# Performance work log

Hardware: AMD Instinct MI355X
Metric: run time of the kernel (lower is better)

The kernel has to match this reference:

```python
import jax, jax.numpy as jnp
import numpy as np
import math

NHID = 32
FEAT_SIZE = 32
FEAT_SIZE_LIST = [16, 32, 32, 32]
SEQ_LEN = len(FEAT_SIZE_LIST)   # 4
N_EDGE_LABELS = 3
NLAYERS = 2
N_GRAPHS = 64
FINAL = SEQ_LEN * NHID          # 128


def _pos_enc(max_len, dim):
    pe = np.zeros((max_len, dim), dtype=np.float32)
    pos = np.arange(max_len, dtype=np.float32)[:, None]
    div = np.exp(np.arange(0, dim, 2, dtype=np.float32) * (-math.log(10000.0) / dim))
    pe[:, 0::2] = np.sin(pos * div)
    pe[:, 1::2] = np.cos(pos * div)
    return jnp.asarray(pe)


def _feature_attention(x, wqkv, w1, b1, w2, b2):
    # x: [N, S*NHID] -> attention over the S feature 'tokens' per node
    N, D = x.shape
    S = D // NHID
    xr = x.reshape(N, S, NHID)
    qkv = jnp.einsum('nsf,fh->nsh', xr, wqkv)          # [N,S,3*NHID]
    q, k, v = jnp.split(qkv, 3, axis=-1)
    att = jax.nn.softmax(jnp.einsum('nsh,nth->nst', q, k) / jnp.sqrt(jnp.asarray(NHID, x.dtype)), axis=-1)
    y = jnp.einsum('nst,nth->nsh', att, v)             # [N,S,NHID]
    y = y + (jax.nn.relu(y @ w1 + b1) @ w2 + b2)       # residual FFN
    return y.reshape(N, -1)


def setup_inputs() -> dict:
    key = jax.random.key(0)
    ks = jax.random.split(key, 16)
    N = 100000
    E = 800000
    inp = {
        'x': jax.random.normal(ks[0], (N, 112), dtype=jnp.float32),
        'edge_index0': jax.random.randint(ks[1], (2, E), 0, N),
        'edge_index1': jax.random.randint(ks[2], (2, E), 0, N),
        'edge_index2': jax.random.randint(ks[3], (2, E), 0, N),
        'batch': jnp.sort(jax.random.randint(ks[4], (N,), 0, N_GRAPHS)),
    }
    s = 0.05
    # FeatureLinear encoder (bias-free)
    inp['W_emb'] = jax.random.normal(ks[5], (FEAT_SIZE, NHID), dtype=jnp.float32) * s
    # Per layer: [root, conv0, conv1, conv2] FeatureAttention params, stacked
    A = 1 + N_EDGE_LABELS
    inp['qkv'] = jax.random.normal(ks[6], (NLAYERS, A, NHID, 3 * NHID), dtype=jnp.float32) * s
    inp['ffn_w1'] = jax.random.normal(ks[7], (NLAYERS, A, NHID, NHID), dtype=jnp.float32) * s
    inp['ffn_b1'] = jnp.zeros((NLAYERS, A, NHID), dtype=jnp.float32)
    inp['ffn_w2'] = jax.random.normal(ks[8], (NLAYERS, A, NHID, NHID), dtype=jnp.float32) * s
    inp['ffn_b2'] = jnp.zeros((NLAYERS, A, NHID), dtype=jnp.float32)
    # Heuristic decoder MLP: 128 -> 128 -> 1
    inp['mlp_w1'] = jax.random.normal(ks[9], (FINAL, FINAL), dtype=jnp.float32) * s
    inp['mlp_b1'] = jnp.zeros((FINAL,), dtype=jnp.float32)
    inp['mlp_w2'] = jax.random.normal(ks[10], (FINAL, 1), dtype=jnp.float32) * s
    inp['mlp_b2'] = jnp.zeros((1,), dtype=jnp.float32)
    return inp


def reference(x, edge_index0, edge_index1, edge_index2, batch,
              W_emb, qkv, ffn_w1, ffn_b1, ffn_w2, ffn_b2,
              mlp_w1, mlp_b1, mlp_w2, mlp_b2):
    N = x.shape[0]
    edge_indices = [edge_index0, edge_index1, edge_index2]

    # padding: split by feat_size_list, right-pad each chunk to FEAT_SIZE
    offs = np.cumsum(FEAT_SIZE_LIST)[:-1].tolist()
    chunks = jnp.split(x, offs, axis=1)
    padded = [jnp.pad(c, ((0, 0), (0, FEAT_SIZE - c.shape[1]))) for c in chunks]
    h = jnp.concatenate(padded, axis=1)                       # [N, SEQ_LEN*FEAT_SIZE]

    # sinusoidal positional encoding over the SEQ_LEN feature tokens
    pe = _pos_enc(10, FEAT_SIZE)[:SEQ_LEN]                    # [SEQ_LEN, FEAT_SIZE]
    h = (h.reshape(N, SEQ_LEN, FEAT_SIZE) + pe[None]).reshape(N, -1)

    # FeatureLinear encoder: per-token linear FEAT_SIZE -> NHID
    h = jnp.einsum('nsf,fh->nsh', h.reshape(N, SEQ_LEN, FEAT_SIZE), W_emb).reshape(N, -1)

    # RGNN layers: root attention + per-edge-label attention->scatter-sum
    for l in range(NLAYERS):
        x_out = _feature_attention(h, qkv[l, 0], ffn_w1[l, 0], ffn_b1[l, 0], ffn_w2[l, 0], ffn_b2[l, 0])
        for e in range(N_EDGE_LABELS):
            a = e + 1
            xt = _feature_attention(h, qkv[l, a], ffn_w1[l, a], ffn_b1[l, a], ffn_w2[l, a], ffn_b2[l, a])
            src, dst = edge_indices[e][0], edge_indices[e][1]
            x_out = x_out + jax.ops.segment_sum(xt[src], dst, num_segments=N)
        h = jax.nn.relu(x_out)

    # global mean pool over graphs
    sums = jax.ops.segment_sum(h, batch, num_segments=N_GRAPHS)
    cnts = jax.ops.segment_sum(jnp.ones((N,), h.dtype), batch, num_segments=N_GRAPHS)
    g = sums / jnp.maximum(cnts, 1.0)[:, None]                # [G, FINAL]

    # heuristic decoder
    out = jax.nn.relu(g @ mlp_w1 + mlp_b1) @ mlp_w2 + mlp_b2  # [G, 1]
    return out.squeeze(1)                                     # [G]
```

## Files before the change

kernel.cpp:

```cpp
#include <hip/hip_runtime.h>
#include <hip/hip_bf16.h>
#include <cstdint>
#include <cstddef>


typedef __attribute__((ext_vector_type(8))) short bf16x8;
typedef __attribute__((ext_vector_type(4))) float f32x4;
typedef __attribute__((ext_vector_type(2))) float f32x2;

#if defined(__has_builtin)
#if __has_builtin(__builtin_amdgcn_cvt_pk_fp8_f32) && __has_builtin(__builtin_amdgcn_cvt_pk_f32_fp8)
#define HW_FP8 1
#endif
#if __has_builtin(__builtin_amdgcn_cvt_pk_bf16_f32)
#define HW_PKBF16 1
#endif
#endif

__device__ inline short f2bf(float f) {
    union { float f; unsigned u; } v; v.f = f;
    unsigned r = (v.u + 0x7FFFu + ((v.u >> 16) & 1u)) >> 16;
    return (short)r;
}
__device__ inline float bf2f(unsigned short b) {
    union { unsigned u; float f; } v; v.u = ((unsigned)b) << 16;
    return v.f;
}
#ifdef HW_PKBF16
typedef __attribute__((ext_vector_type(2))) __bf16 bf16x2_t;
__device__ inline unsigned pk2(float a, float b) {
    union { bf16x2_t v; unsigned u; } c;
    c.v = __builtin_amdgcn_cvt_pk_bf16_f32(a, b);
    return c.u;
}
#else
__device__ inline unsigned pk2(float a, float b) {
    unsigned ua = __float_as_uint(a) + 0x8000u;
    unsigned ub = __float_as_uint(b) + 0x8000u;
    return __builtin_amdgcn_perm(ub, ua, 0x07060302u);
}
#endif

#ifndef HW_FP8
__device__ inline unsigned char f2fp8_sw(float f) {
    unsigned s = (__float_as_uint(f) >> 31) & 1u;
    float a = fminf(fabsf(f), 448.f);
    unsigned char bits;
    if (a < 0.015625f) {
        bits = (unsigned char)__float2int_rn(a * 512.f);
    } else {
        int e; float m = frexpf(a, &e);
        int mf = __float2int_rn(m * 16.f);
        if (mf == 16) { mf = 8; e += 1; }
        int ef = e - 1 + 7;
        if (ef > 15) { ef = 15; mf = 14; }
        bits = (unsigned char)((ef << 3) | (mf & 7));
    }
    return (unsigned char)((s << 7) | bits);
}
__device__ inline float fp82f_sw(unsigned b) {
    int s = (b >> 7) & 1, e = (b >> 3) & 15, m = b & 7;
    float v = e ? ldexpf((float)(8 + m), e - 10) : ldexpf((float)m, -9);
    return s ? -v : v;
}
#endif

__device__ inline unsigned pk4fp8(float v0, float v1, float v2, float v3) {
#ifdef HW_FP8
    int w = __builtin_amdgcn_cvt_pk_fp8_f32(v0, v1, 0, false);
    w = __builtin_amdgcn_cvt_pk_fp8_f32(v2, v3, w, true);
    return (unsigned)w;
#else
    return (unsigned)f2fp8_sw(v0) | ((unsigned)f2fp8_sw(v1) << 8) |
           ((unsigned)f2fp8_sw(v2) << 16) | ((unsigned)f2fp8_sw(v3) << 24);
#endif
}
__device__ inline float2 up2fp8(unsigned short raw) {
#ifdef HW_FP8
    f32x2 f = __builtin_amdgcn_cvt_pk_f32_fp8((int)(unsigned)raw, false);
    return make_float2(f[0], f[1]);
#else
    return make_float2(fp82f_sw(raw & 0xffu), fp82f_sw((raw >> 8) & 0xffu));
#endif
}

__global__ __launch_bounds__(64) void wprep_kernel(
    const float* __restrict__ qkv, const float* __restrict__ fw1,
    const float* __restrict__ fw2, unsigned short* __restrict__ wpack,
    int* __restrict__ bcnt, int* __restrict__ gres,
    float* __restrict__ gsum, float* __restrict__ gcnt)
{
    const int pi = blockIdx.x;
    const int lane = threadIdx.x;
    const int gid = pi * 64 + lane;
    for (int i = gid; i < 256; i += 512) { bcnt[i] = 0; gres[i] = 0; }
    for (int i = gid; i < 64 * 128; i += 512) gsum[i] = 0.f;
    if (gid < 64) gcnt[gid] = 0.f;

    const int q = lane >> 4, m = lane & 15;
    const float* Wq = qkv + (size_t)pi * 32 * 96;
    const float* W1 = fw1 + (size_t)pi * 32 * 32;
    const float* W2 = fw2 + (size_t)pi * 32 * 32;
    unsigned short* dst = wpack + (size_t)pi * 10 * 64 * 8;
#pragma unroll
    for (int ci = 0; ci < 6; ++ci)
#pragma unroll
        for (int j = 0; j < 8; ++j)
            dst[(ci * 64 + lane) * 8 + j] =
                (unsigned short)f2bf(Wq[(q * 8 + j) * 96 + ci * 16 + m]);
#pragma unroll
    for (int t = 0; t < 2; ++t)
#pragma unroll
        for (int j = 0; j < 8; ++j) {
            dst[((6 + t) * 64 + lane) * 8 + j] =
                (unsigned short)f2bf(W1[(q * 8 + j) * 32 + t * 16 + m]);
            dst[((8 + t) * 64 + lane) * 8 + j] =
                (unsigned short)f2bf(W2[(q * 8 + j) * 32 + t * 16 + m]);
        }
}

__global__ __launch_bounds__(128) void enc_kernel(
    const float* __restrict__ x, const float* __restrict__ Wemb,
    unsigned short* __restrict__ h, int N)
{
    __shared__ float sxr[8 * 112];
    __shared__ float spe[128];
    __shared__ float sW[1024];
    const int t = threadIdx.x;
    const int n0 = blockIdx.x * 8;

    {
        int s = t >> 5, f = t & 31;
        int i2 = f >> 1;
        float div = __expf(-(float)(2 * i2) * (logf(10000.0f) / 32.0f));
        float ang = (float)s * div;
        spe[t] = (f & 1) ? cosf(ang) : sinf(ang);
    }
    for (int i = t; i < 1024; i += 128) sW[i] = Wemb[i];
    for (int i = t; i < 8 * 112; i += 128) {
        int n = n0 + i / 112;
        sxr[i] = (n < N) ? x[(size_t)n0 * 112 + i] : 0.f;
    }
    __syncthreads();

    const int ts = t >> 5, c = t & 31;
    const int offs_[4] = {0, 16, 48, 80};
    const int lens_[4] = {16, 32, 32, 32};
    const int off = offs_[ts], len = lens_[ts];

    float acc[8];
#pragma unroll
    for (int i = 0; i < 8; ++i) acc[i] = 0.f;
    float pw = 0.f;
    for (int f = 0; f < 32; ++f) {
        float wv = sW[f * 32 + c];
        float pv = spe[ts * 32 + f];
        pw += pv * wv;
        if (f < len) {
#pragma unroll
            for (int i = 0; i < 8; ++i) acc[i] += sxr[i * 112 + off + f] * wv;
        }
    }
#pragma unroll
    for (int i = 0; i < 8; ++i) {
        int n = n0 + i;
        if (n < N)
            h[(size_t)n * 128 + ts * 32 + c] = (unsigned short)f2bf(acc[i] + pw);
    }
}

#define ATT_WAVES 4
#define WLDS 5376

__global__ __launch_bounds__(256, 3) void attn4_kernel(
    const unsigned short* __restrict__ in,
    unsigned short* __restrict__ outR, unsigned char* __restrict__ out3,
    const unsigned short* __restrict__ wpack,
    const float* __restrict__ fb1, const float* __restrict__ fb2,
    int pibase, int N)
{
    __shared__ char smem[ATT_WAVES * 2 * WLDS];
    const int lane = threadIdx.x & 63;
    const int wave = threadIdx.x >> 6;
    const int q = lane >> 4;
    const int m = lane & 15;

    char* wb0 = smem + wave * (2 * WLDS);

#pragma unroll
    for (int u = 0; u < 2; ++u) {
        int* p32 = (int*)(wb0 + u * WLDS + 4096);
        for (int i = lane; i < 320; i += 64) p32[i] = 0;
    }

    const f32x4 zf = {0.f, 0.f, 0.f, 0.f};
    const int pi = pibase + wave;
    unsigned char* out8 = out3 + (size_t)(wave - 1) * N * 128;

    bf16x8 wqkv[6], w1f[2], w2f[2];
    float b1r[2][4], b2r[2][4];
    {
        const unsigned short* wp = wpack + ((size_t)pi * 10 * 64 + lane) * 8;
#pragma unroll
        for (int ci = 0; ci < 6; ++ci)
            wqkv[ci] = *(const bf16x8*)(wp + ci * 64 * 8);
#pragma unroll
        for (int t = 0; t < 2; ++t) {
            w1f[t] = *(const bf16x8*)(wp + (6 + t) * 64 * 8);
            w2f[t] = *(const bf16x8*)(wp + (8 + t) * 64 * 8);
#pragma unroll
            for (int r = 0; r < 4; ++r) {
                b1r[t][r] = fb1[pi * 32 + 16 * t + q * 4 + r];
                b2r[t][r] = fb2[pi * 32 + 16 * t + q * 4 + r];
            }
        }
    }

    const int nsuper = (N + 7) >> 3;
    for (int stile = blockIdx.x; stile < nsuper; stile += gridDim.x) {
        const int n0 = stile * 8;

        bf16x8 ax[2];
#pragma unroll
        for (int u = 0; u < 2; ++u) {
            bf16x8 a = {0, 0, 0, 0, 0, 0, 0, 0};
            int nm = n0 + 4 * u + (m >> 2);
            if (nm < N)
                a = *(const bf16x8*)(in + (size_t)(n0 + 4 * u) * 128 + m * 32 + q * 8);
            ax[u] = a;
        }

#pragma unroll
        for (int u = 0; u < 2; ++u) {
            char* wbu = wb0 + u * WLDS;
            short* Qb = (short*)(wbu);
            short* Kb = (short*)(wbu + 1280);
            short* VT = (short*)(wbu + 2560);
            short* Pb = (short*)(wbu + 4096);

            f32x4 aQ[2], aK[2], aV[2];
#pragma unroll
            for (int t = 0; t < 2; ++t) {
                aQ[t] = __builtin_amdgcn_mfma_f32_16x16x32_bf16(wqkv[t],     ax[u], zf, 0, 0, 0);
                aK[t] = __builtin_amdgcn_mfma_f32_16x16x32_bf16(wqkv[2 + t], ax[u], zf, 0, 0, 0);
                aV[t] = __builtin_amdgcn_mfma_f32_16x16x32_bf16(ax[u], wqkv[4 + t], zf, 0, 0, 0);
            }
#pragma unroll
            for (int t = 0; t < 2; ++t) {
                uint2 dq, dk, dv;
                dq.x = pk2(aQ[t][0], aQ[t][1]); dq.y = pk2(aQ[t][2], aQ[t][3]);
                dk.x = pk2(aK[t][0], aK[t][1]); dk.y = pk2(aK[t][2], aK[t][3]);
                dv.x = pk2(aV[t][0], aV[t][1]); dv.y = pk2(aV[t][2], aV[t][3]);
                *(uint2*)(Qb + m * 40 + 16 * t + q * 4) = dq;
                *(uint2*)(Kb + m * 40 + 16 * t + q * 4) = dk;
                *(uint2*)(VT + (16 * t + m) * 24 + q * 4) = dv;
            }

            bf16x8 aKf = *(const bf16x8*)(Kb + m * 40 + q * 8);
            bf16x8 bQf = *(const bf16x8*)(Qb + m * 40 + q * 8);
            f32x4 st = __builtin_amdgcn_mfma_f32_16x16x32_bf16(aKf, bQf, zf, 0, 0, 0);

            float v0 = st[0] * 0.1767766952966369f;
            float v1 = st[1] * 0.1767766952966369f;
            float v2 = st[2] * 0.1767766952966369f;
            float v3 = st[3] * 0.1767766952966369f;
            float mx = fmaxf(fmaxf(v0, v1), fmaxf(v2, v3));
            float e0 = __expf(v0 - mx), e1 = __expf(v1 - mx);
            float e2 = __expf(v2 - mx), e3 = __expf(v3 - mx);
            float inv = 1.0f / (e0 + e1 + e2 + e3);
            if (q == (m >> 2)) {
                uint2 dp;
                dp.x = pk2(e0 * inv, e1 * inv);
                dp.y = pk2(e2 * inv, e3 * inv);
                *(uint2*)(Pb + m * 40 + q * 4) = dp;
            }

            f32x4 y[2];
#pragma unroll
            for (int t = 0; t < 2; ++t) {
                bf16x8 aVf = {0, 0, 0, 0, 0, 0, 0, 0};
                bf16x8 bPf = {0, 0, 0, 0, 0, 0, 0, 0};
                if (q < 2) {
                    aVf = *(const bf16x8*)(VT + (16 * t + m) * 24 + q * 8);
                    bPf = *(const bf16x8*)(Pb + m * 40 + q * 8);
                }
                y[t] = __builtin_amdgcn_mfma_f32_16x16x32_bf16(aVf, bPf, zf, 0, 0, 0);
            }
#pragma unroll
            for (int t = 0; t < 2; ++t) {
                uint2 dy;
                dy.x = pk2(y[t][0], y[t][1]); dy.y = pk2(y[t][2], y[t][3]);
                *(uint2*)(Qb + m * 40 + 16 * t + q * 4) = dy;
            }

            bf16x8 bY = *(const bf16x8*)(Qb + m * 40 + q * 8);
            f32x4 z1[2];
#pragma unroll
            for (int t = 0; t < 2; ++t)
                z1[t] = __builtin_amdgcn_mfma_f32_16x16x32_bf16(w1f[t], bY, zf, 0, 0, 0);
#pragma unroll
            for (int t = 0; t < 2; ++t) {
                uint2 dz;
                dz.x = pk2(fmaxf(z1[t][0] + b1r[t][0], 0.f),
                           fmaxf(z1[t][1] + b1r[t][1], 0.f));
                dz.y = pk2(fmaxf(z1[t][2] + b1r[t][2], 0.f),
                           fmaxf(z1[t][3] + b1r[t][3], 0.f));
                *(uint2*)(Kb + m * 40 + 16 * t + q * 4) = dz;
            }

            bf16x8 bZ = *(const bf16x8*)(Kb + m * 40 + q * 8);
            f32x4 o[2];
#pragma unroll
            for (int t = 0; t < 2; ++t)
                o[t] = __builtin_amdgcn_mfma_f32_16x16x32_bf16(w2f[t], bZ, zf, 0, 0, 0);

            if (n0 + 4 * u + (m >> 2) < N) {
                if (wave == 0) {
#pragma unroll
                    for (int t = 0; t < 2; ++t) {
                        uint2 dd;
                        dd.x = pk2(y[t][0] + o[t][0] + b2r[t][0],
                                   y[t][1] + o[t][1] + b2r[t][1]);
                        dd.y = pk2(y[t][2] + o[t][2] + b2r[t][2],
                                   y[t][3] + o[t][3] + b2r[t][3]);
                        *(uint2*)(outR + (size_t)(n0 + 4 * u) * 128 + m * 32 + 16 * t + q * 4) = dd;
                    }
                } else {
#pragma unroll
                    for (int t = 0; t < 2; ++t) {
                        unsigned pw8 = pk4fp8(
                            (y[t][0] + o[t][0] + b2r[t][0]) * 16.f,
                            (y[t][1] + o[t][1] + b2r[t][1]) * 16.f,
                            (y[t][2] + o[t][2] + b2r[t][2]) * 16.f,
                            (y[t][3] + o[t][3] + b2r[t][3]) * 16.f);
                        *(unsigned*)(out8 + (size_t)(n0 + 4 * u) * 128 + m * 32 + 16 * t + q * 4) = pw8;
                    }
                }
            }
        }
    }
}

#define PA_CHUNK 4096
#define PA_SHIFT 9
#define PA_MAXB  256
#define HB_K     16

__global__ __launch_bounds__(256) void histB_kernel(
    const int* __restrict__ e0, const int* __restrict__ e1,
    const int* __restrict__ e2, int* __restrict__ bcnt, int E)
{
    __shared__ int lh[PA_MAXB];
    const int lab = blockIdx.y;
    const int* e = (lab == 0) ? e0 : (lab == 1) ? e1 : e2;
    const int t = threadIdx.x;
    for (int i = t; i < PA_MAXB; i += 256) lh[i] = 0;
    __syncthreads();
    const int base = blockIdx.x * 256 * HB_K;
#pragma unroll
    for (int k = 0; k < HB_K; ++k) {
        int i = base + k * 256 + t;
        if (i < E) atomicAdd(&lh[e[E + i] >> PA_SHIFT], 1);
    }
    __syncthreads();
    for (int i = t; i < PA_MAXB; i += 256)
        if (lh[i]) atomicAdd(&bcnt[i], lh[i]);
}

__global__ __launch_bounds__(256) void bscan_kernel(
    const int* __restrict__ bcnt, int* __restrict__ bbase)
{
    __shared__ int sd[PA_MAXB];
    const int t = threadIdx.x;
    sd[t] = bcnt[t];
    __syncthreads();
    int own = sd[t];
    for (int o = 1; o < 256; o <<= 1) {
        int v = (t >= o) ? sd[t - o] : 0;
        __syncthreads();
        sd[t] += v;
        __syncthreads();
    }
    bbase[t] = sd[t] - own;
}

__global__ __launch_bounds__(256) void placeA_kernel(
    const int* __restrict__ e0, const int* __restrict__ e1, const int* __restrict__ e2,
    const int* __restrict__ bbase, int* __restrict__ gres,
    int2* __restrict__ pairs, int E, int N)
{
    __shared__ int2 sStage[PA_CHUNK];
    __shared__ int sCnt[PA_MAXB], sScan[PA_MAXB], sCur[PA_MAXB], sGB[PA_MAXB];

    const int lab = blockIdx.y;
    const int t = threadIdx.x;
    const int base = blockIdx.x * PA_CHUNK;
    const int* e = (lab == 0) ? e0 : (lab == 1) ? e1 : e2;
    const int srcoff = lab * N;
    const int nbins = (N + (1 << PA_SHIFT) - 1) >> PA_SHIFT;

    for (int i = t; i < PA_MAXB; i += 256) { sCnt[i] = 0; sCur[i] = 0; }
    __syncthreads();

    int msrc[16], mdst[16];
    const int cnt_total = min(PA_CHUNK, E - base);
#pragma unroll
    for (int k = 0; k < 16; ++k) {
        int i = base + k * 256 + t;
        if (i < E) {
            msrc[k] = srcoff + e[i];
            int d = e[E + i];
            mdst[k] = d;
            atomicAdd(&sCnt[d >> PA_SHIFT], 1);
        } else mdst[k] = -1;
    }
    __syncthreads();

    sScan[t] = sCnt[t];
    __syncthreads();
    for (int o = 1; o < 256; o <<= 1) {
        int v = (t >= o) ? sScan[t - o] : 0;
        __syncthreads();
        sScan[t] += v;
        __syncthreads();
    }
    if (t < nbins && sCnt[t] > 0)
        sGB[t] = bbase[t] + atomicAdd(&gres[t], sCnt[t]);
    __syncthreads();

#pragma unroll
    for (int k = 0; k < 16; ++k) {
        if (mdst[k] >= 0) {
            int bin = mdst[k] >> PA_SHIFT;
            int r = atomicAdd(&sCur[bin], 1);
            sStage[(sScan[bin] - sCnt[bin]) + r] = make_int2(msrc[k], mdst[k]);
        }
    }
    __syncthreads();

    for (int i = t; i < cnt_total; i += 256) {
        int2 pr = sStage[i];
        int bin = pr.y >> PA_SHIFT;
        pairs[sGB[bin] + (i - (sScan[bin] - sCnt[bin]))] = pr;
    }
}

__global__ __launch_bounds__(512) void placeB_kernel(
    const int2* __restrict__ pairs, const int* __restrict__ bbase,
    const int* __restrict__ bcnt, int* __restrict__ offs,
    int* __restrict__ csr, int N, int nbins)
{
    __shared__ int sCnt[512], sScan[512], sFill[512];
    const int bin = blockIdx.x;
    const int t = threadIdx.x;
    const int n0 = bin << PA_SHIFT;
    const int n1 = min(n0 + 512, N);
    const int len = n1 - n0;
    const int rb  = bbase[bin];
    const int cnt = bcnt[bin];
    const int2* gp = pairs + rb;

    sCnt[t] = 0; sFill[t] = 0;
    __syncthreads();
    for (int i = t; i < cnt; i += 512)
        atomicAdd(&sCnt[gp[i].y - n0], 1);
    __syncthreads();
    sScan[t] = sCnt[t];
    __syncthreads();
    for (int o = 1; o < 512; o <<= 1) {
        int v = (t >= o) ? sScan[t - o] : 0;
        __syncthreads();
        sScan[t] += v;
        __syncthreads();
    }
    const int excl = sScan[t] - sCnt[t];
    if (t < len) offs[n0 + t] = rb + excl;
    if (bin == nbins - 1 && t == 0) offs[N] = rb + cnt;
    sScan[t] = excl;
    __syncthreads();

    for (int i = t; i < cnt; i += 512) {
        int2 pr = gp[i];
        int ln = pr.y - n0;
        int p = atomicAdd(&sFill[ln], 1);
        csr[rb + sScan[ln] + p] = pr.x;
    }
}

__global__ __launch_bounds__(256) void agg3_kernel(
    const unsigned short* __restrict__ xtR,
    const unsigned char* __restrict__ xt3,
    const int* __restrict__ csr, const int* __restrict__ offs,
    unsigned short* __restrict__ hout, int N)
{
    int w = threadIdx.x >> 6, lane = threadIdx.x & 63;
    int dst = blockIdx.x * 4 + w;
    if (dst >= N) return;

    const ushort2* r2 = (const ushort2*)xtR;
    ushort2 rv = r2[(size_t)dst * 64 + lane];
    float2 a[8];
#pragma unroll
    for (int i = 0; i < 8; ++i) a[i] = make_float2(0.f, 0.f);

    const unsigned short* x8 = (const unsigned short*)xt3;
    const int beg = offs[dst], end = offs[dst + 1];
    int k = beg;
    for (; k + 8 <= end; k += 8) {
        int4 sa = *(const int4*)(csr + k);
        int4 sb = *(const int4*)(csr + k + 4);
        int s[8] = {sa.x, sa.y, sa.z, sa.w, sb.x, sb.y, sb.z, sb.w};
        unsigned short v[8];
#pragma unroll
        for (int i = 0; i < 8; ++i) v[i] = x8[(size_t)s[i] * 64 + lane];
#pragma unroll
        for (int i = 0; i < 8; ++i) {
            float2 f = up2fp8(v[i]);
            a[i].x += f.x; a[i].y += f.y;
        }
    }
    for (; k + 2 <= end; k += 2) {
        unsigned short v0 = x8[(size_t)csr[k] * 64 + lane];
        unsigned short v1 = x8[(size_t)csr[k + 1] * 64 + lane];
        float2 f0 = up2fp8(v0), f1 = up2fp8(v1);
        a[0].x += f0.x; a[0].y += f0.y;
        a[1].x += f1.x; a[1].y += f1.y;
    }
    for (; k < end; ++k) {
        float2 f0 = up2fp8(x8[(size_t)csr[k] * 64 + lane]);
        a[0].x += f0.x; a[0].y += f0.y;
    }
    float sx = ((a[0].x + a[1].x) + (a[2].x + a[3].x)) +
               ((a[4].x + a[5].x) + (a[6].x + a[7].x));
    float sy = ((a[0].y + a[1].y) + (a[2].y + a[3].y)) +
               ((a[4].y + a[5].y) + (a[6].y + a[7].y));
    float fx = bf2f(rv.x) + 0.0625f * sx;
    float fy = bf2f(rv.y) + 0.0625f * sy;
    ((unsigned*)hout)[(size_t)dst * 64 + lane] = pk2(fmaxf(fx, 0.f), fmaxf(fy, 0.f));
}

__global__ __launch_bounds__(256) void pool_kernel(
    const unsigned short* __restrict__ in, const int* __restrict__ batch,
    float* __restrict__ gsum, float* __restrict__ gcnt, int N)
{
    int t = threadIdx.x;
    int j = t & 127, half = t >> 7;
    int n0 = blockIdx.x * 64 + half * 32;
    float acc = 0.f, c = 0.f; int cur = -1;
    for (int i = 0; i < 32; ++i) {
        int n = n0 + i;
        if (n >= N) break;
        int g = batch[n];
        if (g != cur) {
            if (cur >= 0) {
                atomicAdd(&gsum[cur * 128 + j], acc);
                if (j == 0) atomicAdd(&gcnt[cur], c);
            }
            cur = g; acc = 0.f; c = 0.f;
        }
        acc += bf2f(in[(size_t)n * 128 + j]);
        c += 1.f;
    }
    if (cur >= 0) {
        atomicAdd(&gsum[cur * 128 + j], acc);
        if (j == 0) atomicAdd(&gcnt[cur], c);
    }
}

__global__ __launch_bounds__(128) void dec_kernel(
    const float* __restrict__ gsum, const float* __restrict__ gcnt,
    const float* __restrict__ W1, const float* __restrict__ B1,
    const float* __restrict__ W2, const float* __restrict__ B2,
    float* __restrict__ out)
{
    __shared__ float sg[128];
    __shared__ float sh[128];
    int t = threadIdx.x, b = blockIdx.x;
    float cinv = 1.0f / fmaxf(gcnt[b], 1.0f);
    sg[t] = gsum[b * 128 + t] * cinv;
    __syncthreads();
    float acc = B1[t];
    for (int f = 0; f < 128; ++f) acc += sg[f] * W1[f * 128 + t];
    sh[t] = fmaxf(acc, 0.f) * W2[t];
    __syncthreads();
    for (int o = 64; o > 0; o >>= 1) {
        if (t < o) sh[t] += sh[t + o];
        __syncthreads();
    }
    if (t == 0) out[b] = sh[0] + B2[0];
}

extern "C" void kernel_launch(void* const* d_in, const int* in_sizes, int n_in,
                              void* d_out, int out_size, void* d_ws, size_t ws_size,
                              hipStream_t stream)
{
    const float* x    = (const float*)d_in[0];
    const int*   e0   = (const int*)d_in[1];
    const int*   e1   = (const int*)d_in[2];
    const int*   e2   = (const int*)d_in[3];
    const int*   bat  = (const int*)d_in[4];
    const float* Wemb = (const float*)d_in[5];
    const float* qkv  = (const float*)d_in[6];
    const float* fw1  = (const float*)d_in[7];
    const float* fb1  = (const float*)d_in[8];
    const float* fw2  = (const float*)d_in[9];
    const float* fb2  = (const float*)d_in[10];
    const float* mw1  = (const float*)d_in[11];
    const float* mb1  = (const float*)d_in[12];
    const float* mw2  = (const float*)d_in[13];
    const float* mb2  = (const float*)d_in[14];
    const int N = in_sizes[0] / 112;
    const int E = in_sizes[1] / 2;
    float* outp = (float*)d_out;
    (void)n_in; (void)out_size; (void)ws_size;

    char* w = (char*)d_ws;
    auto alloc = [&](size_t bytes) {
        char* p = w; w += (bytes + 255) & ~(size_t)255; return p;
    };
    unsigned short* h0    = (unsigned short*)alloc((size_t)N * 128 * 2);
    unsigned short* h1    = (unsigned short*)alloc((size_t)N * 128 * 2);
    unsigned short* xtR   = (unsigned short*)alloc((size_t)N * 128 * 2);
    unsigned char*  xt3   = (unsigned char*)alloc((size_t)3 * N * 128);
    unsigned short* wpack = (unsigned short*)alloc(8 * 10 * 64 * 8 * 2);
    int*   csr   = (int*)alloc((size_t)3 * E * 4);
    int*   offs  = (int*)alloc((size_t)(N + 1) * 4);
    int*   bcnt  = (int*)alloc(PA_MAXB * 4);
    int*   bbase = (int*)alloc(PA_MAXB * 4);
    int*   gres  = (int*)alloc(PA_MAXB * 4);
    float* gsum  = (float*)alloc(64 * 128 * 4);
    float* gcnt  = (float*)alloc(64 * 4);
    int2* pairs = (int2*)xtR;

    const int nbins = (N + (1 << PA_SHIFT) - 1) >> PA_SHIFT;

    wprep_kernel<<<8, 64, 0, stream>>>(qkv, fw1, fw2, wpack, bcnt, gres, gsum, gcnt);
    enc_kernel<<<(N + 7) / 8, 128, 0, stream>>>(x, Wemb, h0, N);

    histB_kernel<<<dim3((E + 256 * HB_K - 1) / (256 * HB_K), 3), 256, 0, stream>>>(
        e0, e1, e2, bcnt, E);
    bscan_kernel<<<1, 256, 0, stream>>>(bcnt, bbase);
    placeA_kernel<<<dim3((E + PA_CHUNK - 1) / PA_CHUNK, 3), 256, 0, stream>>>(
        e0, e1, e2, bbase, gres, pairs, E, N);
    placeB_kernel<<<nbins, 512, 0, stream>>>(pairs, bbase, bcnt, offs, csr, N, nbins);

    const int ATT_GRID = 768;
    auto run_layer = [&](const unsigned short* lin, unsigned short* lout, int l) {
        attn4_kernel<<<ATT_GRID, 256, 0, stream>>>(
            lin, xtR, xt3, wpack, fb1, fb2, l * 4, N);
        agg3_kernel<<<(N + 3) / 4, 256, 0, stream>>>(xtR, xt3, csr, offs, lout, N);
    };
    run_layer(h0, h1, 0);
    run_layer(h1, h0, 1);

    pool_kernel<<<(N + 63) / 64, 256, 0, stream>>>(h0, bat, gsum, gcnt, N);
    dec_kernel<<<64, 128, 0, stream>>>(gsum, gcnt, mw1, mb1, mw2, mb2, outp);
}
```

Measured before the change: 497.7 us.

## Split wavefront into four edge groups with 8-byte gathers in aggregation

```diff
diff --git a/kernel.cpp b/kernel.cpp
--- a/kernel.cpp
+++ b/kernel.cpp
@@ -84,6 +84,23 @@
 #endif
 }
 
+__device__ inline void acc8(float* a, uint2 v) {
+#ifdef HW_FP8
+    f32x2 f0 = __builtin_amdgcn_cvt_pk_f32_fp8((int)v.x, false);
+    f32x2 f1 = __builtin_amdgcn_cvt_pk_f32_fp8((int)v.x, true);
+    f32x2 f2 = __builtin_amdgcn_cvt_pk_f32_fp8((int)v.y, false);
+    f32x2 f3 = __builtin_amdgcn_cvt_pk_f32_fp8((int)v.y, true);
+    a[0] += f0[0]; a[1] += f0[1]; a[2] += f1[0]; a[3] += f1[1];
+    a[4] += f2[0]; a[5] += f2[1]; a[6] += f3[0]; a[7] += f3[1];
+#else
+    unsigned b0 = v.x, b1 = v.y;
+#pragma unroll
+    for (int j = 0; j < 4; ++j) a[j]     += fp82f_sw((b0 >> (8 * j)) & 0xffu);
+#pragma unroll
+    for (int j = 0; j < 4; ++j) a[4 + j] += fp82f_sw((b1 >> (8 * j)) & 0xffu);
+#endif
+}
+
 __global__ __launch_bounds__(64) void wprep_kernel(
     const float* __restrict__ qkv, const float* __restrict__ fw1,
     const float* __restrict__ fw2, unsigned short* __restrict__ wpack,
@@ -493,50 +510,63 @@
     const int* __restrict__ csr, const int* __restrict__ offs,
     unsigned short* __restrict__ hout, int N)
 {
-    int w = threadIdx.x >> 6, lane = threadIdx.x & 63;
-    int dst = blockIdx.x * 4 + w;
+    const int w = threadIdx.x >> 6, lane = threadIdx.x & 63;
+    const int dst = blockIdx.x * 4 + w;
     if (dst >= N) return;
 
-    const ushort2* r2 = (const ushort2*)xtR;
-    ushort2 rv = r2[(size_t)dst * 64 + lane];
-    float2 a[8];
-#pragma unroll
-    for (int i = 0; i < 8; ++i) a[i] = make_float2(0.f, 0.f);
-
-    const unsigned short* x8 = (const unsigned short*)xt3;
+    const int g = lane >> 4;
+    const unsigned fl8 = (unsigned)(lane & 15) << 3;
+
+    bf16x8 rv = *(const bf16x8*)(xtR + (size_t)dst * 128 + fl8);
+
+    float a[8];
+#pragma unroll
+    for (int i = 0; i < 8; ++i) a[i] = 0.f;
+
     const int beg = offs[dst], end = offs[dst + 1];
-    int k = beg;
-    for (; k + 8 <= end; k += 8) {
-        int4 sa = *(const int4*)(csr + k);
-        int4 sb = *(const int4*)(csr + k + 4);
-        int s[8] = {sa.x, sa.y, sa.z, sa.w, sb.x, sb.y, sb.z, sb.w};
-        unsigned short v[8];
-#pragma unroll
-        for (int i = 0; i < 8; ++i) v[i] = x8[(size_t)s[i] * 64 + lane];
-#pragma unroll
-        for (int i = 0; i < 8; ++i) {
-            float2 f = up2fp8(v[i]);
-            a[i].x += f.x; a[i].y += f.y;
-        }
-    }
-    for (; k + 2 <= end; k += 2) {
-        unsigned short v0 = x8[(size_t)csr[k] * 64 + lane];
-        unsigned short v1 = x8[(size_t)csr[k + 1] * 64 + lane];
-        float2 f0 = up2fp8(v0), f1 = up2fp8(v1);
-        a[0].x += f0.x; a[0].y += f0.y;
-        a[1].x += f1.x; a[1].y += f1.y;
-    }
-    for (; k < end; ++k) {
-        float2 f0 = up2fp8(x8[(size_t)csr[k] * 64 + lane]);
-        a[0].x += f0.x; a[0].y += f0.y;
-    }
-    float sx = ((a[0].x + a[1].x) + (a[2].x + a[3].x)) +
-               ((a[4].x + a[5].x) + (a[6].x + a[7].x));
-    float sy = ((a[0].y + a[1].y) + (a[2].y + a[3].y)) +
-               ((a[4].y + a[5].y) + (a[6].y + a[7].y));
-    float fx = bf2f(rv.x) + 0.0625f * sx;
-    float fy = bf2f(rv.y) + 0.0625f * sy;
-    ((unsigned*)hout)[(size_t)dst * 64 + lane] = pk2(fmaxf(fx, 0.f), fmaxf(fy, 0.f));
+    if (beg < end) {
+        const int last = end - 1;
+        int e0 = beg + g, e1 = beg + 4 + g;
+        int c0 = csr[min(e0, last)];
+        int c1 = csr[min(e1, last)];
+        c0 = (e0 > last) ? -1 : c0;
+        c1 = (e1 > last) ? -1 : c1;
+        for (int k = beg; k < end; k += 8) {
+            const int nk = k + 8;
+            unsigned s0 = (unsigned)max(c0, 0);
+            unsigned s1 = (unsigned)max(c1, 0);
+            uint2 v0 = *(const uint2*)(xt3 + (s0 << 7) + fl8);
+            uint2 v1 = *(const uint2*)(xt3 + (s1 << 7) + fl8);
+            int ne0 = nk + g, ne1 = nk + 4 + g;
+            int n0_ = csr[min(ne0, last)];
+            int n1_ = csr[min(ne1, last)];
+            n0_ = (ne0 > last) ? -1 : n0_;
+            n1_ = (ne1 > last) ? -1 : n1_;
+            v0.x = (c0 < 0) ? 0u : v0.x;  v0.y = (c0 < 0) ? 0u : v0.y;
+            v1.x = (c1 < 0) ? 0u : v1.x;  v1.y = (c1 < 0) ? 0u : v1.y;
+            acc8(a, v0);
+            acc8(a, v1);
+            c0 = n0_; c1 = n1_;
+        }
+    }
+
+#pragma unroll
+    for (int i = 0; i < 8; ++i) {
+        a[i] += __shfl_xor(a[i], 16);
+        a[i] += __shfl_xor(a[i], 32);
+    }
+
+    if (g == 0) {
+        unsigned r[4];
+#pragma unroll
+        for (int t = 0; t < 4; ++t) {
+            float f0 = bf2f((unsigned short)rv[2 * t])     + 0.0625f * a[2 * t];
+            float f1 = bf2f((unsigned short)rv[2 * t + 1]) + 0.0625f * a[2 * t + 1];
+            r[t] = pk2(fmaxf(f0, 0.f), fmaxf(f1, 0.f));
+        }
+        uint4 st = make_uint4(r[0], r[1], r[2], r[3]);
+        *(uint4*)(hout + (size_t)dst * 128 + fl8) = st;
+    }
 }
 
 __global__ __launch_bounds__(256) void pool_kernel(
```

Measured after the change: 471.9 us. -5.2%, faster.
